# Kernel tuning notes

Hardware: AMD Instinct MI355X
Metric: run time of the kernel (lower is better)

## Reference

```python
import jax, jax.numpy as jnp
import numpy as np

B, N, D, G = 32, 1024, 512, 32  # batch, set size, in_features, num_gaussians


def setup_inputs() -> dict:
    key = jax.random.key(0)
    k1, k2 = jax.random.split(key)
    minibatch = jax.random.normal(k1, (B, N, D), dtype=jnp.float32)
    # xavier_uniform for Linear(D -> G)
    limit = float(np.sqrt(6.0 / (D + G)))
    W_pi = jax.random.uniform(k2, (G, D), dtype=jnp.float32, minval=-limit, maxval=limit)
    b_pi = jnp.zeros((G,), dtype=jnp.float32)
    return {"minibatch": minibatch, "W_pi": W_pi, "b_pi": b_pi}


def reference(minibatch, W_pi, b_pi):
    d = minibatch.shape[-1]
    o = d // 2
    # mixture weights per (batch, sample): softmax over gaussian axis
    logits = jnp.einsum('bnd,gd->bng', minibatch, W_pi) + b_pi  # [B,N,G]
    pi = jax.nn.softmax(logits, axis=2)
    mu = minibatch[:, :, :o]        # [B,N,O]
    sigma = minibatch[:, :, -o:]    # [B,N,O]
    weights = jnp.mean(pi, axis=1)  # [B,G]
    denom = jnp.sum(pi, axis=1)     # [B,G]
    # weighted first moment -> locs (vectorized over all gaussians at once)
    m1 = jnp.einsum('bng,bno->bgo', pi, mu)                 # [B,G,O]
    locs = m1 / denom[:, :, None]                            # [B,G,O]
    # weighted E[mu^2 + sigma^2]; variance = E[mu^2+sigma^2] - locs^2
    # (identical math to sum(pi*((locs-mu)^2 + sigma^2))/sum(pi))
    m2 = jnp.einsum('bng,bno->bgo', pi, mu * mu + sigma * sigma)
    var = m2 / denom[:, :, None] - locs * locs
    scales = jnp.sqrt(jnp.maximum(var, 0.0))                 # [B,G,O]
    return weights, scales, locs
```

## Files before the change

### kernel.cpp

```cpp
#include <hip/hip_runtime.h>
#include <stdint.h>

#define B_ 32
#define N_ 1024
#define D_ 512
#define G_ 32

typedef __attribute__((ext_vector_type(8))) short short8;
typedef __attribute__((ext_vector_type(4))) float f32x4;
union U4S8 { uint4 u; short8 s; };

#define WS_DN  2097152
#define WS_WF  2105344

__device__ inline uint32_t pack_bf16x2(float a, float b) {
  uint32_t ua = __float_as_uint(a);
  uint32_t ub = __float_as_uint(b);
  ua += 0x7FFFu + ((ua >> 16) & 1u);
  ub += 0x7FFFu + ((ub >> 16) & 1u);
  return (ua >> 16) | (ub & 0xFFFF0000u);
}
__device__ inline uint16_t bf16r(float a) {
  uint32_t u = __float_as_uint(a);
  u += 0x7FFFu + ((u >> 16) & 1u);
  return (uint16_t)(u >> 16);
}
__device__ inline float bflo(uint32_t u) { return __uint_as_float(u << 16); }
__device__ inline float bfhi(uint32_t u) { return __uint_as_float(u & 0xFFFF0000u); }
__device__ inline int slot_of(int o) { return (o & 7) ^ ((o >> 3) & 3); }

__global__ __launch_bounds__(256) void mdn_k0(
    const float* __restrict__ W, float* ws)
{
  int s = blockIdx.x * 256 + threadIdx.x;
  int g = s >> 6;
  int d0 = (s & 63) * 8;
  const float4* src = (const float4*)(W + g * D_ + d0);
  float4 f0 = src[0], f1 = src[1];
  int ks = d0 >> 5, ksub = (d0 >> 3) & 3;
  uint4 v;
  v.x = pack_bf16x2(f0.x, f0.y); v.y = pack_bf16x2(f0.z, f0.w);
  v.z = pack_bf16x2(f1.x, f1.y); v.w = pack_bf16x2(f1.z, f1.w);
  ((uint4*)(ws + WS_WF))[(ks * 4 + ksub) * 32 + g] = v;
}

__global__ __launch_bounds__(512, 2) void mdn_kf(
    const float* __restrict__ x, const float* __restrict__ bpi, float* ws)
{
  __shared__ uint32_t XT[32768];
  __shared__ uint32_t PT[2048];
  __shared__ float wpart[8][32];

  const int t = threadIdx.x;
  const int bid = blockIdx.x;
  const int b = bid >> 3;
  const int n0 = (bid & 7) * 128;
  const int w = t >> 6;
  const int lane = t & 63;
  const int l15 = lane & 15, l4 = lane >> 4;

  const float* abase =
      x + ((size_t)(b * N_ + n0 + w * 16 + l15)) * D_ + l4 * 8;
  const uint4* wf4 = (const uint4*)(ws + WS_WF);
  const int r = w * 16 + l15;

  f32x4 acc0 = {0.f, 0.f, 0.f, 0.f};
  f32x4 acc1 = {0.f, 0.f, 0.f, 0.f};

  #pragma unroll
  for (int h = 0; h < 2; ++h) {
    float4 fa[8], fb[8];
    #pragma unroll
    for (int k = 0; k < 8; ++k) {
      const float* s = abase + (h * 8 + k) * 32;
      fa[k] = *(const float4*)s; fb[k] = *(const float4*)(s + 4);
    }
    #pragma unroll
    for (int k = 0; k < 8; ++k) {
      int ks = h * 8 + k;
      U4S8 a;
      a.u.x = pack_bf16x2(fa[k].x, fa[k].y);
      a.u.y = pack_bf16x2(fa[k].z, fa[k].w);
      a.u.z = pack_bf16x2(fb[k].x, fb[k].y);
      a.u.w = pack_bf16x2(fb[k].z, fb[k].w);
      {
        int d0 = l4 * 8 + ks * 32;
        unsigned xtb = (unsigned)((d0 >> 4) * 4096 + r * 32 + (d0 & 15) * 2);
        *(uint4*)((char*)XT + xtb) = a.u;
      }
      int wi = (ks * 4 + l4) * 32 + l15;
      U4S8 w0, w1;
      w0.u = wf4[wi];
      w1.u = wf4[wi + 16];
      acc0 = __builtin_amdgcn_mfma_f32_16x16x32_bf16(a.s, w0.s, acc0, 0, 0, 0);
      acc1 = __builtin_amdgcn_mfma_f32_16x16x32_bf16(a.s, w1.s, acc1, 0, 0, 0);
    }
  }

  float bs0 = bpi[l15], bs1 = bpi[16 + l15];
  float pi0[4], pi1[4];
  float dsum0 = 0.f, dsum1 = 0.f;
  #pragma unroll
  for (int j = 0; j < 4; ++j) {
    float v0 = acc0[j] + bs0, v1 = acc1[j] + bs1;
    float m = fmaxf(v0, v1);
    m = fmaxf(m, __shfl_xor(m, 1));
    m = fmaxf(m, __shfl_xor(m, 2));
    m = fmaxf(m, __shfl_xor(m, 4));
    m = fmaxf(m, __shfl_xor(m, 8));
    float e0 = __expf(v0 - m), e1 = __expf(v1 - m);
    float s = e0 + e1;
    s += __shfl_xor(s, 1); s += __shfl_xor(s, 2);
    s += __shfl_xor(s, 4); s += __shfl_xor(s, 8);
    float inv = 1.0f / s;
    pi0[j] = e0 * inv; pi1[j] = e1 * inv;
    dsum0 += pi0[j];   dsum1 += pi1[j];
  }
  dsum0 += __shfl_xor(dsum0, 16); dsum0 += __shfl_xor(dsum0, 32);
  dsum1 += __shfl_xor(dsum1, 16); dsum1 += __shfl_xor(dsum1, 32);
  if (lane < 16) { wpart[w][lane] = dsum0; wpart[w][16 + lane] = dsum1; }

  {
    uint16_t* p16 = (uint16_t*)PT;
    int rbase = w * 16 + l4 * 4;
    int g0 = l15, g1 = 16 + l15;
    int s0 = slot_of(g0) << 3, s1 = slot_of(g1) << 3;
    #pragma unroll
    for (int j = 0; j < 4; ++j) {
      int rr = rbase + j;
      p16[g0 * 128 + (rr ^ s0)] = bf16r(pi0[j]);
      p16[g1 * 128 + (rr ^ s1)] = bf16r(pi1[j]);
    }
  }
  __syncthreads();

  if (t < 32) {
    float s = 0.f;
    #pragma unroll
    for (int ww = 0; ww < 8; ++ww) s += wpart[ww][t];
    ws[WS_DN + (size_t)bid * 32 + t] = s;
  }

  f32x4 m1a[2][2] = {{{0.f,0.f,0.f,0.f},{0.f,0.f,0.f,0.f}},
                     {{0.f,0.f,0.f,0.f},{0.f,0.f,0.f,0.f}}};
  f32x4 m2a[2][2] = {{{0.f,0.f,0.f,0.f},{0.f,0.f,0.f,0.f}},
                     {{0.f,0.f,0.f,0.f},{0.f,0.f,0.f,0.f}}};
  const int gA0 = l15, gA1 = 16 + l15;
  const int sA0 = slot_of(gA0) << 2, sA1 = slot_of(gA1) << 2;
  const unsigned xtb0 = (unsigned)(uintptr_t)XT;

  #pragma unroll
  for (int ksi = 0; ksi < 4; ++ksi) {
    int rofs = ksi * 16 + l4 * 4;
    U4S8 a0, a1;
    a0.u = *(const uint4*)(PT + gA0 * 64 + (rofs ^ sA0));
    a1.u = *(const uint4*)(PT + gA1 * 64 + (rofs ^ sA1));
    const unsigned rowb = (unsigned)(ksi * 1024 + l4 * 256 + l15 * 8);
    #pragma unroll
    for (int ot = 0; ot < 2; ++ot) {
      unsigned am = xtb0 + (unsigned)((w * 2 + ot) * 4096) + rowb;
      unsigned as = am + 16 * 4096;
      uint64_t q0, q1, q2, q3;
      asm volatile("ds_read_b64_tr_b16 %0, %1" : "=v"(q0) : "v"(am));
      asm volatile("ds_read_b64_tr_b16 %0, %1 offset:128" : "=v"(q1) : "v"(am));
      asm volatile("ds_read_b64_tr_b16 %0, %1" : "=v"(q2) : "v"(as));
      asm volatile("ds_read_b64_tr_b16 %0, %1 offset:128" : "=v"(q3) : "v"(as));
      asm volatile("s_waitcnt lgkmcnt(0)" ::: "memory");
      __builtin_amdgcn_sched_barrier(0);
      U4S8 Bm, Bs;
      Bm.u.x = (uint32_t)q0; Bm.u.y = (uint32_t)(q0 >> 32);
      Bm.u.z = (uint32_t)q1; Bm.u.w = (uint32_t)(q1 >> 32);
      Bs.u.x = (uint32_t)q2; Bs.u.y = (uint32_t)(q2 >> 32);
      Bs.u.z = (uint32_t)q3; Bs.u.w = (uint32_t)(q3 >> 32);
      uint32_t bm[4] = {Bm.u.x, Bm.u.y, Bm.u.z, Bm.u.w};
      uint32_t sw[4] = {Bs.u.x, Bs.u.y, Bs.u.z, Bs.u.w};
      U4S8 B2;
      uint32_t b2w[4];
      #pragma unroll
      for (int i = 0; i < 4; ++i) {
        float lo = bflo(bm[i]) * bflo(bm[i]) + bflo(sw[i]) * bflo(sw[i]);
        float hi = bfhi(bm[i]) * bfhi(bm[i]) + bfhi(sw[i]) * bfhi(sw[i]);
        b2w[i] = pack_bf16x2(lo, hi);
      }
      B2.u.x = b2w[0]; B2.u.y = b2w[1]; B2.u.z = b2w[2]; B2.u.w = b2w[3];
      m1a[0][ot] = __builtin_amdgcn_mfma_f32_16x16x32_bf16(a0.s, Bm.s, m1a[0][ot], 0, 0, 0);
      m1a[1][ot] = __builtin_amdgcn_mfma_f32_16x16x32_bf16(a1.s, Bm.s, m1a[1][ot], 0, 0, 0);
      m2a[0][ot] = __builtin_amdgcn_mfma_f32_16x16x32_bf16(a0.s, B2.s, m2a[0][ot], 0, 0, 0);
      m2a[1][ot] = __builtin_amdgcn_mfma_f32_16x16x32_bf16(a1.s, B2.s, m2a[1][ot], 0, 0, 0);
    }
  }

  uint32_t* dst = (uint32_t*)ws + (size_t)bid * 8192;
  #pragma unroll
  for (int gt = 0; gt < 2; ++gt) {
    #pragma unroll
    for (int ot = 0; ot < 2; ++ot) {
      int col = w * 32 + ot * 16 + l15;
      #pragma unroll
      for (int jj = 0; jj < 4; ++jj) {
        int g = gt * 16 + l4 * 4 + jj;
        dst[g * 256 + col] = pack_bf16x2(m1a[gt][ot][jj], m2a[gt][ot][jj]);
      }
    }
  }
}

__global__ __launch_bounds__(256) void mdn_k3(
    const float* __restrict__ ws, float* __restrict__ out)
{
  __shared__ float dnm[G_];
  const int blk = blockIdx.x;
  const int b = blk >> 3, oc = blk & 7;
  const int t = threadIdx.x;
  if (t < G_) {
    float s = 0.f;
    #pragma unroll
    for (int c = 0; c < 8; ++c) s += ws[WS_DN + (size_t)(b * 8 + c) * 32 + t];
    dnm[t] = s;
    if (oc == 0) out[b * G_ + t] = s * (1.0f / 1024.0f);
  }
  __syncthreads();
  const int g = t >> 3;
  const int o = oc * 32 + (t & 7) * 4;
  const uint32_t* wsU = (const uint32_t*)ws;
  float4 m1 = make_float4(0.f, 0.f, 0.f, 0.f);
  float4 m2 = make_float4(0.f, 0.f, 0.f, 0.f);
  #pragma unroll
  for (int c = 0; c < 8; ++c) {
    const uint32_t* p = wsU + (size_t)(b * 8 + c) * 8192 + g * 256 + o;
    uint4 v = *(const uint4*)p;
    m1.x += bflo(v.x); m1.y += bflo(v.y); m1.z += bflo(v.z); m1.w += bflo(v.w);
    m2.x += bfhi(v.x); m2.y += bfhi(v.y); m2.z += bfhi(v.z); m2.w += bfhi(v.w);
  }
  float inv = 1.0f / dnm[g];
  float4 lc = make_float4(m1.x * inv, m1.y * inv, m1.z * inv, m1.w * inv);
  float4 sc;
  sc.x = sqrtf(fmaxf(m2.x * inv - lc.x * lc.x, 0.f));
  sc.y = sqrtf(fmaxf(m2.y * inv - lc.y * lc.y, 0.f));
  sc.z = sqrtf(fmaxf(m2.z * inv - lc.z * lc.z, 0.f));
  sc.w = sqrtf(fmaxf(m2.w * inv - lc.w * lc.w, 0.f));
  float* scales = out + 1024;
  float* locs = out + 1024 + 262144;
  int oi = ((b * G_ + g) << 8) + o;
  *(float4*)(scales + oi) = sc;
  *(float4*)(locs + oi) = lc;
}

extern "C" void kernel_launch(void* const* d_in, const int* in_sizes, int n_in,
                              void* d_out, int out_size, void* d_ws, size_t ws_size,
                              hipStream_t stream)
{
  const float* x = (const float*)d_in[0];
  const float* W = (const float*)d_in[1];
  const float* bpi = (const float*)d_in[2];
  float* out = (float*)d_out;
  float* ws = (float*)d_ws;
  hipLaunchKernelGGL(mdn_k0, dim3(8), dim3(256), 0, stream, W, ws);
  hipLaunchKernelGGL(mdn_kf, dim3(256), dim3(512), 0, stream, x, bpi, ws);
  hipLaunchKernelGGL(mdn_k3, dim3(256), dim3(256), 0, stream, ws, out);
}
```

Before: 29.98 us.

## Fuse final reduction into main kernel via last-block atomic counter

```diff
diff --git a/kernel.cpp b/kernel.cpp
--- a/kernel.cpp
+++ b/kernel.cpp
@@ -12,6 +12,7 @@
 
 #define WS_DN  2097152
 #define WS_WF  2105344
+#define WS_CNT 2113536
 
 __device__ inline uint32_t pack_bf16x2(float a, float b) {
   uint32_t ua = __float_as_uint(a);
@@ -33,6 +34,8 @@
     const float* __restrict__ W, float* ws)
 {
   int s = blockIdx.x * 256 + threadIdx.x;
+  if (blockIdx.x == 0 && threadIdx.x < 32)
+    ((uint32_t*)(ws + WS_CNT))[threadIdx.x] = 0u;
   int g = s >> 6;
   int d0 = (s & 63) * 8;
   const float4* src = (const float4*)(W + g * D_ + d0);
@@ -45,11 +48,14 @@
 }
 
 __global__ __launch_bounds__(512, 2) void mdn_kf(
-    const float* __restrict__ x, const float* __restrict__ bpi, float* ws)
+    const float* __restrict__ x, const float* __restrict__ bpi, float* ws,
+    float* __restrict__ out)
 {
   __shared__ uint32_t XT[32768];
   __shared__ uint32_t PT[2048];
   __shared__ float wpart[8][32];
+  __shared__ int lastflag;
+  __shared__ float dnm[G_];
 
   const int t = threadIdx.x;
   const int bid = blockIdx.x;
@@ -203,47 +209,56 @@
       }
     }
   }
-}
-
-__global__ __launch_bounds__(256) void mdn_k3(
-    const float* __restrict__ ws, float* __restrict__ out)
-{
-  __shared__ float dnm[G_];
-  const int blk = blockIdx.x;
-  const int b = blk >> 3, oc = blk & 7;
-  const int t = threadIdx.x;
-  if (t < G_) {
+
+  __threadfence();
+  __syncthreads();
+  if (t == 0) {
+    uint32_t old = atomicAdd(((uint32_t*)(ws + WS_CNT)) + b, 1u);
+    lastflag = (old == 7u);
+  }
+  __syncthreads();
+  if (!lastflag) return;
+  __threadfence();
+
+  if (t < 32) {
     float s = 0.f;
     #pragma unroll
     for (int c = 0; c < 8; ++c) s += ws[WS_DN + (size_t)(b * 8 + c) * 32 + t];
     dnm[t] = s;
-    if (oc == 0) out[b * G_ + t] = s * (1.0f / 1024.0f);
-  }
-  __syncthreads();
-  const int g = t >> 3;
-  const int o = oc * 32 + (t & 7) * 4;
-  const uint32_t* wsU = (const uint32_t*)ws;
-  float4 m1 = make_float4(0.f, 0.f, 0.f, 0.f);
-  float4 m2 = make_float4(0.f, 0.f, 0.f, 0.f);
-  #pragma unroll
-  for (int c = 0; c < 8; ++c) {
-    const uint32_t* p = wsU + (size_t)(b * 8 + c) * 8192 + g * 256 + o;
-    uint4 v = *(const uint4*)p;
-    m1.x += bflo(v.x); m1.y += bflo(v.y); m1.z += bflo(v.z); m1.w += bflo(v.w);
-    m2.x += bfhi(v.x); m2.y += bfhi(v.y); m2.z += bfhi(v.z); m2.w += bfhi(v.w);
-  }
-  float inv = 1.0f / dnm[g];
-  float4 lc = make_float4(m1.x * inv, m1.y * inv, m1.z * inv, m1.w * inv);
-  float4 sc;
-  sc.x = sqrtf(fmaxf(m2.x * inv - lc.x * lc.x, 0.f));
-  sc.y = sqrtf(fmaxf(m2.y * inv - lc.y * lc.y, 0.f));
-  sc.z = sqrtf(fmaxf(m2.z * inv - lc.z * lc.z, 0.f));
-  sc.w = sqrtf(fmaxf(m2.w * inv - lc.w * lc.w, 0.f));
-  float* scales = out + 1024;
-  float* locs = out + 1024 + 262144;
-  int oi = ((b * G_ + g) << 8) + o;
-  *(float4*)(scales + oi) = sc;
-  *(float4*)(locs + oi) = lc;
+    out[b * G_ + t] = s * (1.0f / 1024.0f);
+  }
+  __syncthreads();
+
+  {
+    const uint32_t* wsU = (const uint32_t*)ws;
+    int g = t >> 4;
+    int o0 = (t & 15) * 16;
+    float inv = 1.0f / dnm[g];
+    float* scales = out + 1024;
+    float* locs = out + 1024 + 262144;
+    #pragma unroll
+    for (int q = 0; q < 4; ++q) {
+      int o = o0 + q * 4;
+      float4 m1 = make_float4(0.f, 0.f, 0.f, 0.f);
+      float4 m2 = make_float4(0.f, 0.f, 0.f, 0.f);
+      #pragma unroll
+      for (int c = 0; c < 8; ++c) {
+        const uint32_t* p = wsU + (size_t)(b * 8 + c) * 8192 + g * 256 + o;
+        uint4 v = *(const uint4*)p;
+        m1.x += bflo(v.x); m1.y += bflo(v.y); m1.z += bflo(v.z); m1.w += bflo(v.w);
+        m2.x += bfhi(v.x); m2.y += bfhi(v.y); m2.z += bfhi(v.z); m2.w += bfhi(v.w);
+      }
+      float4 lc = make_float4(m1.x * inv, m1.y * inv, m1.z * inv, m1.w * inv);
+      float4 sc;
+      sc.x = sqrtf(fmaxf(m2.x * inv - lc.x * lc.x, 0.f));
+      sc.y = sqrtf(fmaxf(m2.y * inv - lc.y * lc.y, 0.f));
+      sc.z = sqrtf(fmaxf(m2.z * inv - lc.z * lc.z, 0.f));
+      sc.w = sqrtf(fmaxf(m2.w * inv - lc.w * lc.w, 0.f));
+      int oi = ((b * G_ + g) << 8) + o;
+      *(float4*)(scales + oi) = sc;
+      *(float4*)(locs + oi) = lc;
+    }
+  }
 }
 
 extern "C" void kernel_launch(void* const* d_in, const int* in_sizes, int n_in,
@@ -256,6 +271,5 @@
   float* out = (float*)d_out;
   float* ws = (float*)d_ws;
   hipLaunchKernelGGL(mdn_k0, dim3(8), dim3(256), 0, stream, W, ws);
-  hipLaunchKernelGGL(mdn_kf, dim3(256), dim3(512), 0, stream, x, bpi, ws);
-  hipLaunchKernelGGL(mdn_k3, dim3(256), dim3(256), 0, stream, ws, out);
-}
+  hipLaunchKernelGGL(mdn_kf, dim3(256), dim3(512), 0, stream, x, bpi, ws, out);
+}
```

After: 102.5 us. 3.42x slower.
